# Kernel optimization log

Hardware: AMD Instinct MI355X
Metric: run time of the kernel (lower is better)

## Reference

```python
import jax, jax.numpy as jnp
import numpy as np

BS, M, CLIP_DIM = 64, 1000, 512
D = 512
N_WAYS = 20
N_Z = 8


def setup_inputs() -> dict:
    key = jax.random.key(0)
    ks = jax.random.split(key, 16)
    s = 0.02
    inp = {
        "x_context": jax.random.normal(ks[0], (BS, M, CLIP_DIM), jnp.float32),
        "y_context": jax.random.randint(ks[1], (BS, M), 0, N_WAYS),
        "x_query": jax.random.normal(ks[2], (BS, M, CLIP_DIM), jnp.float32),
        # image_proj
        "Wp": jax.random.normal(ks[3], (CLIP_DIM, D), jnp.float32) * s,
        "bp": jnp.zeros((D,), jnp.float32),
        # aggregator: Linear(d,d) -> GELU -> Linear(d,2d)
        "Wa1": jax.random.normal(ks[4], (D, D), jnp.float32) * s,
        "ba1": jnp.zeros((D,), jnp.float32),
        "Wa2": jax.random.normal(ks[5], (D, 2 * D), jnp.float32) * s,
        "ba2": jnp.zeros((2 * D,), jnp.float32),
        # decoder: Linear(d,d) -> GELU -> Linear(d,d)
        "Wd1": jax.random.normal(ks[6], (D, D), jnp.float32) * s,
        "bd1": jnp.zeros((D,), jnp.float32),
        "Wd2": jax.random.normal(ks[7], (D, D), jnp.float32) * s,
        "bd2": jnp.zeros((D,), jnp.float32),
    }
    return inp


def reference(x_context, y_context, x_query, Wp, bp, Wa1, ba1, Wa2, ba2, Wd1, bd1, Wd2, bd2):
    # project image embeddings: [bs, M, clip_dim] -> [bs, M, d]
    xc = x_context @ Wp + bp
    xq = x_query @ Wp + bp

    # encode_context_per_class: per-class masked sum == one-hot segment-sum
    # (original loops over classes doing (x*mask).sum(dim=1))
    oh = jax.nn.one_hot(y_context, N_WAYS, dtype=xc.dtype)  # [bs, M, N]
    r_C = jnp.einsum('bmn,bmd->bnd', oh, xc)  # [bs, N, d]

    # knowledge is None -> k = zeros; combined = relu(r + 0)
    combined = jax.nn.relu(r_C)
    h = jax.nn.gelu(combined @ Wa1 + ba1, approximate=False)
    stats = h @ Wa2 + ba2  # [bs, N, 2d]
    mu, scale_raw = stats[..., :D], stats[..., D:]
    scale = 0.01 + 0.99 * jax.nn.softplus(scale_raw)

    # eval path: sample n_z from q(z|C) via reparameterization
    eps = jax.random.normal(jax.random.key(42), (N_Z,) + mu.shape, mu.dtype)
    z_samples = mu[None] + scale[None] * eps  # [n_z, bs, N, d]

    # decode: class weight vectors then inner product with queries
    W = jax.nn.gelu(z_samples @ Wd1 + bd1, approximate=False) @ Wd2 + bd2
    logits = jnp.einsum('bqd,sbnd->sbqn', xq, W)  # [n_z, bs, Q*N, N]
    return logits, z_samples, mu, scale
```

## Files before the change

kernel.cpp:

```cpp
#include <hip/hip_runtime.h>
#include <hip/hip_bf16.h>
#include <stdint.h>


typedef __attribute__((ext_vector_type(8))) short short8;
typedef __attribute__((ext_vector_type(4))) float f32x4;

__device__ __forceinline__ float gelu_f(float x) {
    return 0.5f * x * (1.0f + erff(x * 0.70710678118654752440f));
}
__device__ __forceinline__ float softplus_f(float x) {
    return fmaxf(x, 0.0f) + log1pf(expf(-fabsf(x)));
}
__device__ __forceinline__ uint32_t cvt2(float a, float b) {
    __hip_bfloat162 h;
    h.x = __float2bfloat16(a);
    h.y = __float2bfloat16(b);
    uint32_t u; __builtin_memcpy(&u, &h, 4); return u;
}
__device__ __forceinline__ unsigned short f2bfu(float f) {
    __hip_bfloat16 h = __float2bfloat16(f);
    unsigned short u; __builtin_memcpy(&u, &h, 2); return u;
}
__device__ __forceinline__ float bfu2f(unsigned short u) {
    uint32_t v = (uint32_t)u << 16; float f; __builtin_memcpy(&f, &v, 4); return f;
}

__device__ __forceinline__ void threefry2x32(uint32_t k0, uint32_t k1,
                                             uint32_t x0, uint32_t x1,
                                             uint32_t& o0, uint32_t& o1) {
    uint32_t ks[3] = {k0, k1, k0 ^ k1 ^ 0x1BD11BDAu};
    x0 += ks[0]; x1 += ks[1];
    const uint32_t rot[8] = {13,15,26,6,17,29,16,24};
#pragma unroll
    for (int i = 0; i < 5; i++) {
#pragma unroll
        for (int j = 0; j < 4; j++) {
            uint32_t r = rot[(i & 1) * 4 + j];
            x0 += x1;
            x1 = (x1 << r) | (x1 >> (32 - r));
            x1 ^= x0;
        }
        x0 += ks[(i + 1) % 3];
        x1 += ks[(i + 2) % 3] + (uint32_t)(i + 1);
    }
    o0 = x0; o1 = x1;
}

__device__ __forceinline__ float bits_to_normal(uint32_t b) {
    float f = __uint_as_float((b >> 9) | 0x3F800000u) - 1.0f;
    const float lo = __uint_as_float(0xBF7FFFFFu);
    float u = fmaxf(lo, f * 2.0f + lo);
    return 1.41421356237309504880f * erfinvf(u);
}

__global__ __launch_bounds__(256) void po_k(
    const float* __restrict__ Wp, const float* __restrict__ Wa1,
    const float* __restrict__ Wa2, const float* __restrict__ Wd1,
    const float* __restrict__ Wd2, const float* __restrict__ bp,
    const float* __restrict__ bd2, const int* __restrict__ y,
    const float* __restrict__ xc,
    unsigned short* __restrict__ WpTb, unsigned short* __restrict__ Wa1Tb,
    unsigned short* __restrict__ Wa2Tb, unsigned short* __restrict__ WdT1b,
    unsigned short* __restrict__ Gtb,
    float* __restrict__ bv, float* __restrict__ w2bp,
    float* __restrict__ c0, float* __restrict__ cnt,
    float* __restrict__ Apart)
{
    __shared__ __align__(16) char sm[24576];
    __shared__ int lc[256];
    __shared__ float ws4[4];
    const int f = blockIdx.x;
    const int tid = threadIdx.x;

    if (f < 320) {
        float (*T)[65] = reinterpret_cast<float(*)[65]>(sm);
        const float* src; unsigned short* dst; int C, t, xb, yb;
        if (f < 64)       { src = Wp;  dst = WpTb;  C = 512;  t = f;       xb = t & 7;  yb = t >> 3; }
        else if (f < 128) { src = Wa1; dst = Wa1Tb; C = 512;  t = f - 64;  xb = t & 7;  yb = t >> 3; }
        else if (f < 256) { src = Wa2; dst = Wa2Tb; C = 1024; t = f - 128; xb = t & 15; yb = t >> 4; }
        else              { src = Wd1; dst = WdT1b; C = 512;  t = f - 256; xb = t & 7;  yb = t >> 3; }
        const int r0 = yb * 64, cc0 = xb * 64;
        const int rr = tid >> 4, cc = (tid & 15) * 4;
#pragma unroll
        for (int l = 0; l < 4; l++) {
            int row = rr + l * 16;
            float4 v = *(const float4*)&src[(size_t)(r0 + row) * C + cc0 + cc];
            T[row][cc] = v.x; T[row][cc+1] = v.y; T[row][cc+2] = v.z; T[row][cc+3] = v.w;
        }
        __syncthreads();
#pragma unroll
        for (int l = 0; l < 4; l++) {
            int n = rr + l * 16;
            uint2 u;
            u.x = cvt2(T[cc][n], T[cc+1][n]);
            u.y = cvt2(T[cc+2][n], T[cc+3][n]);
            *(uint2*)&dst[(size_t)(cc0 + n) * 512 + r0 + cc] = u;
        }
    } else if (f < 576) {
        const float* W = (f < 448) ? Wp : Wd2;
        const float* v = (f < 448) ? bd2 : bp;
        float* o = (f < 448) ? bv : w2bp;
        int t = (f < 448) ? f - 320 : f - 448;
        int wave = tid >> 6, lane = tid & 63;
        int r = t * 4 + wave;
        const float* row = W + (size_t)r * 512 + lane * 8;
        float4 x0 = *(const float4*)row;
        float4 x1 = *(const float4*)(row + 4);
        float4 v0 = *(const float4*)&v[lane * 8];
        float4 v1 = *(const float4*)&v[lane * 8 + 4];
        float s = x0.x*v0.x + x0.y*v0.y + x0.z*v0.z + x0.w*v0.w
                + x1.x*v1.x + x1.y*v1.y + x1.z*v1.z + x1.w*v1.w;
#pragma unroll
        for (int off = 32; off > 0; off >>= 1) s += __shfl_down(s, off, 64);
        if (lane == 0) o[r] = s;
    } else if (f == 576) {
        float s = bp[tid] * bd2[tid] + bp[tid + 256] * bd2[tid + 256];
#pragma unroll
        for (int off = 32; off > 0; off >>= 1) s += __shfl_down(s, off, 64);
        int wave = tid >> 6, lane = tid & 63;
        if (lane == 0) ws4[wave] = s;
        __syncthreads();
        if (tid == 0) c0[0] = ws4[0] + ws4[1] + ws4[2] + ws4[3];
    } else if (f < 641) {
        int b = f - 577;
        if (tid < 32) lc[tid] = 0;
        __syncthreads();
        for (int m = tid; m < 1000; m += 256)
            atomicAdd(&lc[y[b * 1000 + m]], 1);
        __syncthreads();
        if (tid < 20) cnt[b * 20 + tid] = (float)lc[tid];
    } else if (f < 673) {
        unsigned short* As = (unsigned short*)sm;
        unsigned short* Bs = (unsigned short*)(sm + 8192);
        const int g = f - 641;
        const int lane = tid & 63, w = tid >> 6;
        const int row0 = (g >> 2) * 64, col0 = (g & 3) * 128;
        f32x4 acc[4][2] = {};
        for (int k0 = 0; k0 < 512; k0 += 64) {
            {
                int row = tid >> 2, cs = (tid & 3) * 16;
                int swz = (row & 7) << 4;
                const float* src = Wp + (size_t)(row0 + row) * 512 + k0 + cs;
#pragma unroll
                for (int j = 0; j < 2; j++) {
                    float4 v0 = *(const float4*)(src + j * 8);
                    float4 v1 = *(const float4*)(src + j * 8 + 4);
                    uint4 u;
                    u.x = cvt2(v0.x, v0.y); u.y = cvt2(v0.z, v0.w);
                    u.z = cvt2(v1.x, v1.y); u.w = cvt2(v1.z, v1.w);
                    *(uint4*)((char*)As + row * 128 + (((cs + j * 8) * 2) ^ swz)) = u;
                }
            }
            {
                int row = tid >> 1, cs = (tid & 1) * 32;
                int swz = (row & 7) << 4;
                const float* src = Wd2 + (size_t)(col0 + row) * 512 + k0 + cs;
#pragma unroll
                for (int j = 0; j < 4; j++) {
                    float4 v0 = *(const float4*)(src + j * 8);
                    float4 v1 = *(const float4*)(src + j * 8 + 4);
                    uint4 u;
                    u.x = cvt2(v0.x, v0.y); u.y = cvt2(v0.z, v0.w);
                    u.z = cvt2(v1.x, v1.y); u.w = cvt2(v1.z, v1.w);
                    *(uint4*)((char*)Bs + row * 128 + (((cs + j * 8) * 2) ^ swz)) = u;
                }
            }
            __syncthreads();
#pragma unroll
            for (int ks = 0; ks < 2; ks++) {
                short8 a[4], bb[2];
#pragma unroll
                for (int mi = 0; mi < 4; mi++) {
                    int r = mi * 16 + (lane & 15);
                    a[mi] = *(const short8*)((const char*)As + r * 128 +
                              (((ks * 32 + (lane >> 4) * 8) * 2) ^ ((r & 7) << 4)));
                }
#pragma unroll
                for (int ni = 0; ni < 2; ni++) {
                    int n = w * 32 + ni * 16 + (lane & 15);
                    bb[ni] = *(const short8*)((const char*)Bs + n * 128 +
                              (((ks * 32 + (lane >> 4) * 8) * 2) ^ ((n & 7) << 4)));
                }
#pragma unroll
                for (int mi = 0; mi < 4; mi++)
#pragma unroll
                    for (int ni = 0; ni < 2; ni++)
                        acc[mi][ni] = __builtin_amdgcn_mfma_f32_16x16x32_bf16(a[mi], bb[ni], acc[mi][ni], 0, 0, 0);
            }
            __syncthreads();
        }
#pragma unroll
        for (int mi = 0; mi < 4; mi++)
#pragma unroll
            for (int ni = 0; ni < 2; ni++) {
                int c = col0 + w * 32 + ni * 16 + (lane & 15);
#pragma unroll
                for (int j = 0; j < 4; j++) {
                    int r = row0 + mi * 16 + (lane >> 4) * 4 + j;
                    Gtb[(size_t)r * 512 + c] = f2bfu(acc[mi][ni][j]);
                }
            }
    } else {
        unsigned short* Xs = (unsigned short*)sm;
        int* ys = lc;
        const int f2 = f - 673;
        const int chb = (f2 & 3) * 128;
        const int mc = (f2 >> 2) & 3;
        const int b = f2 >> 4;
        const int m00 = mc * 256;
        const int lane = tid & 63, w = tid >> 6;
        const int chs = w * 32;
        {
            int mg = m00 + tid;
            ys[tid] = (mg < 1000) ? y[b * 1000 + mg] : -1;
        }
        f32x4 acc[2][2] = {};
        for (int step = 0; step < 4; step++) {
            const int k0 = step * 64;
            int m = m00 + k0 + lane; if (m > 999) m = 999;
            const float* src = xc + ((size_t)b * 1000 + m) * 512 + chb + chs;
            float x[32];
#pragma unroll
            for (int j8 = 0; j8 < 8; j8++) {
                float4 v = *(const float4*)(src + j8 * 4);
                x[j8*4+0]=v.x; x[j8*4+1]=v.y; x[j8*4+2]=v.z; x[j8*4+3]=v.w;
            }
            __syncthreads();
#pragma unroll
            for (int j = 0; j < 32; j++) {
                int ch = chs + j;
                *(unsigned short*)((char*)Xs + ch * 128 + ((lane * 2) ^ ((ch & 7) << 4)))
                    = f2bfu(x[j]);
            }
            __syncthreads();
#pragma unroll
            for (int ks = 0; ks < 2; ks++) {
                int kb = ks * 32 + (lane >> 4) * 8;
                int4 yv0 = *(const int4*)&ys[k0 + kb];
                int4 yv1 = *(const int4*)&ys[k0 + kb + 4];
                int ya[8] = {yv0.x, yv0.y, yv0.z, yv0.w, yv1.x, yv1.y, yv1.z, yv1.w};
                short8 a[2];
#pragma unroll
                for (int mi = 0; mi < 2; mi++) {
                    int cls = mi * 16 + (lane & 15);
#pragma unroll
                    for (int e = 0; e < 8; e++)
                        a[mi][e] = (short)((ya[e] == cls) ? 0x3F80 : 0);
                }
                short8 bb[2];
#pragma unroll
                for (int ni = 0; ni < 2; ni++) {
                    int ch = chs + ni * 16 + (lane & 15);
                    bb[ni] = *(const short8*)((const char*)Xs + ch * 128 +
                               ((kb * 2) ^ ((ch & 7) << 4)));
                }
#pragma unroll
                for (int mi = 0; mi < 2; mi++)
#pragma unroll
                    for (int ni = 0; ni < 2; ni++)
                        acc[mi][ni] = __builtin_amdgcn_mfma_f32_16x16x32_bf16(a[mi], bb[ni], acc[mi][ni], 0, 0, 0);
            }
        }
        float* dst = Apart + (size_t)mc * 655360;
#pragma unroll
        for (int mi = 0; mi < 2; mi++) {
#pragma unroll
            for (int ni = 0; ni < 2; ni++) {
                int ch = chb + chs + ni * 16 + (lane & 15);
#pragma unroll
                for (int j = 0; j < 4; j++) {
                    int cls = mi * 16 + (lane >> 4) * 4 + j;
                    if (cls < 20)
                        dst[((size_t)b * 20 + cls) * 512 + ch] = acc[mi][ni][j];
                }
            }
        }
    }
}

template <int EPI, int MT, int A4>
__global__ __launch_bounds__(256) void gm2_k(const unsigned short* __restrict__ Abf,
                                             const unsigned short* __restrict__ Bbf,
                                             const float* __restrict__ bias,
                                             const float* __restrict__ extra,
                                             unsigned short* __restrict__ C0,
                                             float* __restrict__ F0,
                                             float* __restrict__ F1,
                                             int Nn) {
    __shared__ unsigned short As[MT * 64];
    __shared__ unsigned short Bs[128 * 64];
    const int tid = threadIdx.x;
    const int lane = tid & 63, w = tid >> 6;
    const int row0 = blockIdx.y * MT, col0 = blockIdx.x * 128;
    f32x4 acc[MT / 16][2] = {};
    for (int k0 = 0; k0 < 512; k0 += 64) {
        if constexpr (MT == 64) {
            int row = tid >> 2, cs = (tid & 3) * 16;
            int swz = (row & 7) << 4;
            const unsigned short* src = Abf + (size_t)(row0 + row) * 512 + k0 + cs;
#pragma unroll
            for (int j = 0; j < 2; j++) {
                uint4 u = *(const uint4*)(src + j * 8);
                *(uint4*)((char*)As + row * 128 + (((cs + j * 8) * 2) ^ swz)) = u;
            }
        } else {
            int row = tid >> 3, cs = (tid & 7) * 8;
            int swz = (row & 7) << 4;
            uint4 u;
            if constexpr (A4) {
                const float* p = (const float*)Abf + (size_t)(row0 + row) * 512 + k0 + cs;
                float4 s0 = *(const float4*)p;
                float4 s1 = *(const float4*)(p + 4);
#pragma unroll
                for (int q = 1; q < 4; q++) {
                    const float* pp = p + (size_t)q * 655360;
                    float4 v0 = *(const float4*)pp, v1 = *(const float4*)(pp + 4);
                    s0.x += v0.x; s0.y += v0.y; s0.z += v0.z; s0.w += v0.w;
                    s1.x += v1.x; s1.y += v1.y; s1.z += v1.z; s1.w += v1.w;
                }
                u.x = cvt2(s0.x, s0.y); u.y = cvt2(s0.z, s0.w);
                u.z = cvt2(s1.x, s1.y); u.w = cvt2(s1.z, s1.w);
            } else {
                u = *(const uint4*)(Abf + (size_t)(row0 + row) * 512 + k0 + cs);
            }
            *(uint4*)((char*)As + row * 128 + ((cs * 2) ^ swz)) = u;
        }
        {
            int row = tid >> 1, cs = (tid & 1) * 32;
            int swz = (row & 7) << 4;
            const unsigned short* src = Bbf + (size_t)(col0 + row) * 512 + k0 + cs;
#pragma unroll
            for (int j = 0; j < 4; j++) {
                uint4 u = *(const uint4*)(src + j * 8);
                *(uint4*)((char*)Bs + row * 128 + (((cs + j * 8) * 2) ^ swz)) = u;
            }
        }
        __syncthreads();
#pragma unroll
        for (int ks = 0; ks < 2; ks++) {
            short8 a[MT / 16], bb[2];
#pragma unroll
            for (int mi = 0; mi < MT / 16; mi++) {
                int r = mi * 16 + (lane & 15);
                a[mi] = *(const short8*)((const char*)As + r * 128 +
                          (((ks * 32 + (lane >> 4) * 8) * 2) ^ ((r & 7) << 4)));
            }
#pragma unroll
            for (int ni = 0; ni < 2; ni++) {
                int n = w * 32 + ni * 16 + (lane & 15);
                bb[ni] = *(const short8*)((const char*)Bs + n * 128 +
                          (((ks * 32 + (lane >> 4) * 8) * 2) ^ ((n & 7) << 4)));
            }
#pragma unroll
            for (int mi = 0; mi < MT / 16; mi++)
#pragma unroll
                for (int ni = 0; ni < 2; ni++)
                    acc[mi][ni] = __builtin_amdgcn_mfma_f32_16x16x32_bf16(a[mi], bb[ni], acc[mi][ni], 0, 0, 0);
        }
        __syncthreads();
    }
#pragma unroll
    for (int mi = 0; mi < MT / 16; mi++) {
#pragma unroll
        for (int ni = 0; ni < 2; ni++) {
            int c = col0 + w * 32 + ni * 16 + (lane & 15);
            float bvv = bias ? bias[c] : 0.f;
#pragma unroll
            for (int j = 0; j < 4; j++) {
                int r = row0 + mi * 16 + (lane >> 4) * 4 + j;
                float v = acc[mi][ni][j];
                if (EPI == 0) {
                    v += bvv;
                    C0[(size_t)r * Nn + c] = f2bfu(v);
                } else if (EPI == 1) {
                    v += extra[r] * bvv;
                    C0[(size_t)r * Nn + c] = f2bfu(fmaxf(v, 0.f));
                } else if (EPI == 2) {
                    C0[(size_t)r * Nn + c] = f2bfu(gelu_f(v + bvv));
                } else {
                    v += bvv;
                    if (c < 512) F0[(size_t)r * 512 + c] = v;
                    else F1[(size_t)r * 512 + (c - 512)] = 0.01f + 0.99f * softplus_f(v);
                }
            }
        }
    }
}

__global__ __launch_bounds__(256) void z2_k(const float* __restrict__ mu,
                                            const float* __restrict__ sc,
                                            float* __restrict__ z,
                                            unsigned short* __restrict__ zb) {
    const uint32_t NH = 2621440u;
    uint32_t i = blockIdx.x * 256u + threadIdx.x;
    if (i >= NH) return;
    uint32_t t0 = 2u * i;
    uint32_t o0, o1, p0, p1;
    threefry2x32(0u, 42u, 0u, t0, o0, o1);
    threefry2x32(0u, 42u, 0u, t0 + 1u, p0, p1);
    uint32_t r0 = t0 % 655360u;
    float2 mv = *(const float2*)&mu[r0];
    float2 sv = *(const float2*)&sc[r0];
    float z0 = mv.x + sv.x * bits_to_normal(o0 ^ o1);
    float z1 = mv.y + sv.y * bits_to_normal(p0 ^ p1);
    float2 zo; zo.x = z0; zo.y = z1;
    *(float2*)&z[t0] = zo;
    *(uint32_t*)&zb[t0] = cvt2(z0, z1);
}

__global__ __launch_bounds__(512) void wgv_k(const unsigned short* __restrict__ zb,
                                             const unsigned short* __restrict__ Wd1T,
                                             const unsigned short* __restrict__ Gt,
                                             const float* __restrict__ bd1,
                                             const float* __restrict__ bv,
                                             const float* __restrict__ w2bp,
                                             const float* __restrict__ c0,
                                             unsigned short* __restrict__ Vbf,
                                             float* __restrict__ beta) {
    __shared__ unsigned short Wg[64 * 512];
    __shared__ unsigned short As[64 * 64];
    const int r0 = blockIdx.x * 64;
    const int tid = threadIdx.x, lane = tid & 63, w = tid >> 6;
    const int col0 = w * 64;

    f32x4 acc[4][4] = {};
    for (int k0 = 0; k0 < 512; k0 += 64) {
        {
            int row = tid >> 3, cs = (tid & 7) * 8;
            int swz = (row & 7) << 4;
            uint4 u = *(const uint4*)(zb + (size_t)(r0 + row) * 512 + k0 + cs);
            *(uint4*)((char*)As + row * 128 + ((cs * 2) ^ swz)) = u;
        }
        __syncthreads();
#pragma unroll
        for (int ks = 0; ks < 2; ks++) {
            int kb = ks * 32 + (lane >> 4) * 8;
            short8 a[4], bb[4];
#pragma unroll
            for (int mi = 0; mi < 4; mi++) {
                int r = mi * 16 + (lane & 15);
                a[mi] = *(const short8*)((const char*)As + r * 128 +
                          ((kb * 2) ^ ((r & 7) << 4)));
            }
#pragma unroll
            for (int ni = 0; ni < 4; ni++) {
                int n = col0 + ni * 16 + (lane & 15);
                bb[ni] = *(const short8*)(Wd1T + (size_t)n * 512 + k0 + kb);
            }
#pragma unroll
            for (int mi = 0; mi < 4; mi++)
#pragma unroll
                for (int ni = 0; ni < 4; ni++)
                    acc[mi][ni] = __builtin_amdgcn_mfma_f32_16x16x32_bf16(a[mi], bb[ni], acc[mi][ni], 0, 0, 0);
        }
        __syncthreads();
    }
#pragma unroll
    for (int mi = 0; mi < 4; mi++) {
#pragma unroll
        for (int ni = 0; ni < 4; ni++) {
            int c = col0 + ni * 16 + (lane & 15);
            float bvv = bd1[c];
#pragma unroll
            for (int j = 0; j < 4; j++) {
                int r = mi * 16 + (lane >> 4) * 4 + j;
                float v = gelu_f(acc[mi][ni][j] + bvv);
                *(unsigned short*)((char*)Wg + r * 1024 + ((c * 2) ^ ((r & 7) << 4)))
                    = f2bfu(v);
            }
        }
    }
    __syncthreads();

    {
        int row = tid >> 3, p = tid & 7;
        const char* base = (const char*)Wg + row * 1024;
        int swz = (row & 7) << 4;
        float s = 0.f;
#pragma unroll
        for (int j = 0; j < 64; j++) {
            int c = p * 64 + j;
            s += bfu2f(*(const unsigned short*)(base + ((c * 2) ^ swz))) * w2bp[c];
        }
#pragma unroll
        for (int off = 4; off > 0; off >>= 1) s += __shfl_down(s, off, 64);
        if (p == 0) beta[r0 + row] = s + c0[0];
    }

    f32x4 acc2[4][4] = {};
    for (int k0 = 0; k0 < 512; k0 += 64) {
#pragma unroll
        for (int ks = 0; ks < 2; ks++) {
            int kb = ks * 32 + (lane >> 4) * 8;
            short8 a[4], bb[4];
#pragma unroll
            for (int mi = 0; mi < 4; mi++) {
                int r = mi * 16 + (lane & 15);
                a[mi] = *(const short8*)((const char*)Wg + r * 1024 +
                          (((k0 + kb) * 2) ^ ((r & 7) << 4)));
            }
#pragma unroll
            for (int ni = 0; ni < 4; ni++) {
                int n = col0 + ni * 16 + (lane & 15);
                bb[ni] = *(const short8*)(Gt + (size_t)n * 512 + k0 + kb);
            }
#pragma unroll
            for (int mi = 0; mi < 4; mi++)
#pragma unroll
                for (int ni = 0; ni < 4; ni++)
                    acc2[mi][ni] = __builtin_amdgcn_mfma_f32_16x16x32_bf16(a[mi], bb[ni], acc2[mi][ni], 0, 0, 0);
        }
    }
#pragma unroll
    for (int mi = 0; mi < 4; mi++) {
#pragma unroll
        for (int ni = 0; ni < 4; ni++) {
            int c = col0 + ni * 16 + (lane & 15);
            float bvv = bv[c];
#pragma unroll
            for (int j = 0; j < 4; j++) {
                int r = r0 + mi * 16 + (lane >> 4) * 4 + j;
                Vbf[(size_t)r * 512 + c] = f2bfu(acc2[mi][ni][j] + bvv);
            }
        }
    }
}

__global__ __launch_bounds__(512) void logits_mfma4_k(const float* __restrict__ Xq,
                                                      const unsigned short* __restrict__ Vb,
                                                      const float* __restrict__ beta,
                                                      float* __restrict__ out) {
    __shared__ unsigned short Vs[2][160 * 64];
    __shared__ float bs[160];
    const int u = blockIdx.x + 8 * blockIdx.y;
    const int xcd = u & 7, idx = u >> 3;
    const int b = (idx & 7) * 8 + xcd;
    const int qh = idx >> 3;
    const int tid = threadIdx.x, lane = tid & 63, w = tid >> 6;
    const int wq = w >> 1, wn = w & 1;

    if (tid < 160) {
        int s = tid / 20, n = tid - s * 20;
        bs[tid] = beta[(size_t)(s * 64 + b) * 20 + n];
    }

    auto stageV = [&](int buf, int k0) {
        for (int c = tid; c < 640; c += 512) {
            int row = c >> 2, off = (c & 3) * 32;
            int sdiv = row / 20;
            int row_g = row + sdiv * 1260 + b * 20;
            const unsigned short* src = Vb + (size_t)row_g * 512 + k0 + (c & 3) * 16;
            uint4 u0 = *(const uint4*)src;
            uint4 u1 = *(const uint4*)(src + 8);
            int swz = (row & 7) << 4;
            char* base = (char*)&Vs[buf][0] + row * 128;
            *(uint4*)(base + (off ^ swz)) = u0;
            *(uint4*)(base + ((off + 16) ^ swz)) = u1;
        }
    };

    const int klane = (lane >> 4) * 8;
    const float* xp[2];
    int qb[2];
#pragma unroll
    for (int qs = 0; qs < 2; qs++) {
        qb[qs] = qh * 128 + wq * 32 + qs * 16;
        int qr = qb[qs] + (lane & 15);
        if (qr > 999) qr = 999;
        xp[qs] = Xq + ((size_t)b * 1000 + qr) * 512 + klane;
    }
    int vrow[5], vswz[5];
#pragma unroll
    for (int nf = 0; nf < 5; nf++) {
        int rr = wn * 80 + nf * 16 + (lane & 15);
        vrow[nf] = rr * 128;
        vswz[nf] = (rr & 7) << 4;
    }

    stageV(0, 0);
    __syncthreads();

    f32x4 acc[2][5] = {};
    int cur = 0;
    for (int step = 0; step < 8; step++) {
        const int k0 = step * 64;
        if (step < 7) stageV(cur ^ 1, k0 + 64);
        const char* vbase = (const char*)&Vs[cur][0];
#pragma unroll
        for (int ks = 0; ks < 2; ks++) {
            int kb = (ks * 32 + klane) * 2;
            short8 bf[5];
#pragma unroll
            for (int nf = 0; nf < 5; nf++)
                bf[nf] = *(const short8*)(vbase + vrow[nf] + (kb ^ vswz[nf]));
            short8 af[2];
#pragma unroll
            for (int qs = 0; qs < 2; qs++) {
                const float* p = xp[qs] + k0 + ks * 32;
                float4 v0 = *(const float4*)p;
                float4 v1 = *(const float4*)(p + 4);
                uint4 uu;
                uu.x = cvt2(v0.x, v0.y); uu.y = cvt2(v0.z, v0.w);
                uu.z = cvt2(v1.x, v1.y); uu.w = cvt2(v1.z, v1.w);
                __builtin_memcpy(&af[qs], &uu, 16);
            }
#pragma unroll
            for (int qs = 0; qs < 2; qs++)
#pragma unroll
                for (int nf = 0; nf < 5; nf++)
                    acc[qs][nf] = __builtin_amdgcn_mfma_f32_16x16x32_bf16(af[qs], bf[nf], acc[qs][nf], 0, 0, 0);
        }
        __syncthreads();
        cur ^= 1;
    }

#pragma unroll
    for (int nf = 0; nf < 5; nf++) {
        int rl = wn * 80 + nf * 16 + (lane & 15);
        int s = rl / 20, n = rl - s * 20;
        float bb = bs[rl];
        size_t ob = (size_t)(s * 64 + b) * 20000;
#pragma unroll
        for (int qs = 0; qs < 2; qs++) {
#pragma unroll
            for (int j = 0; j < 4; j++) {
                int q = qb[qs] + (lane >> 4) * 4 + j;
                if (q < 1000)
                    out[ob + (size_t)q * 20 + n] = acc[qs][nf][j] + bb;
            }
        }
    }
}

extern "C" void kernel_launch(void* const* d_in, const int* in_sizes, int n_in,
                              void* d_out, int out_size, void* d_ws, size_t ws_size,
                              hipStream_t stream) {
    const float* x_context = (const float*)d_in[0];
    const int*   y_context = (const int*)d_in[1];
    const float* x_query   = (const float*)d_in[2];
    const float* Wp  = (const float*)d_in[3];
    const float* bp  = (const float*)d_in[4];
    const float* Wa1 = (const float*)d_in[5];
    const float* ba1 = (const float*)d_in[6];
    const float* Wa2 = (const float*)d_in[7];
    const float* ba2 = (const float*)d_in[8];
    const float* Wd1 = (const float*)d_in[9];
    const float* bd1 = (const float*)d_in[10];
    const float* Wd2 = (const float*)d_in[11];
    const float* bd2 = (const float*)d_in[12];

    float* out    = (float*)d_out;
    float* logits = out;
    float* z      = out + 10240000;
    float* mu     = out + 15482880;
    float* sc     = out + 16138240;

    float* ws   = (float*)d_ws;
    float* cnt  = ws;
    float* beta = cnt + 1280;
    float* bv   = beta + 10240;
    float* w2bp = bv + 512;
    float* c0   = w2bp + 512;
    unsigned short* WpTb  = (unsigned short*)(c0 + 63);
    unsigned short* Wa1Tb = WpTb + 262144;
    unsigned short* Wa2Tb = Wa1Tb + 262144;
    unsigned short* WdT1b = Wa2Tb + 524288;
    unsigned short* Gtb   = WdT1b + 262144;
    unsigned short* combb = Gtb + 262144;
    unsigned short* hb    = combb + 655360;
    unsigned short* zb    = hb + 655360;
    unsigned short* Vbf   = zb + 5242880;
    float* big = (float*)(Vbf + 5242880);

    po_k<<<dim3(1697), 256, 0, stream>>>(Wp, Wa1, Wa2, Wd1, Wd2, bp, bd2, y_context,
                                         x_context,
                                         WpTb, Wa1Tb, Wa2Tb, WdT1b, Gtb,
                                         bv, w2bp, c0, cnt, big);
    gm2_k<1, 32, 1><<<dim3(4, 40), 256, 0, stream>>>((const unsigned short*)big, WpTb, bp, cnt, combb, nullptr, nullptr, 512);
    gm2_k<2, 32, 0><<<dim3(4, 40), 256, 0, stream>>>(combb, Wa1Tb, ba1, nullptr, hb, nullptr, nullptr, 512);
    gm2_k<3, 32, 0><<<dim3(8, 40), 256, 0, stream>>>(hb, Wa2Tb, ba2, nullptr, nullptr, mu, sc, 1024);
    z2_k<<<dim3(10240), 256, 0, stream>>>(mu, sc, z, zb);
    wgv_k<<<dim3(160), 512, 0, stream>>>(zb, WdT1b, Gtb, bd1, bv, w2bp, c0, Vbf, beta);
    logits_mfma4_k<<<dim3(8, 64), 512, 0, stream>>>(x_query, Vbf, beta, logits);
}
```

Measured before the change: 216.1 us.

## Fuse projection, aggregator MLP and stats GEMMs into one chained kernel

Replaces three separate gm2_k launches (projection+relu, Wa1+GELU, Wa2+softplus) with a single chain_k kernel that keeps each 64-row tile's intermediate activations in shared memory across all three GEMMs. This removes two kernel launches and the global round trips of the combined and hidden bf16 buffers. In exchange only 20 blocks run, so the GPU is heavily underused, and B operands are read directly from global memory rather than staged in LDS.

```diff
diff --git a/kernel.cpp b/kernel.cpp
--- a/kernel.cpp
+++ b/kernel.cpp
@@ -279,37 +279,29 @@
     }
 }
 
-template <int EPI, int MT, int A4>
-__global__ __launch_bounds__(256) void gm2_k(const unsigned short* __restrict__ Abf,
-                                             const unsigned short* __restrict__ Bbf,
-                                             const float* __restrict__ bias,
-                                             const float* __restrict__ extra,
-                                             unsigned short* __restrict__ C0,
-                                             float* __restrict__ F0,
-                                             float* __restrict__ F1,
-                                             int Nn) {
-    __shared__ unsigned short As[MT * 64];
-    __shared__ unsigned short Bs[128 * 64];
-    const int tid = threadIdx.x;
-    const int lane = tid & 63, w = tid >> 6;
-    const int row0 = blockIdx.y * MT, col0 = blockIdx.x * 128;
-    f32x4 acc[MT / 16][2] = {};
-    for (int k0 = 0; k0 < 512; k0 += 64) {
-        if constexpr (MT == 64) {
-            int row = tid >> 2, cs = (tid & 3) * 16;
-            int swz = (row & 7) << 4;
-            const unsigned short* src = Abf + (size_t)(row0 + row) * 512 + k0 + cs;
-#pragma unroll
-            for (int j = 0; j < 2; j++) {
-                uint4 u = *(const uint4*)(src + j * 8);
-                *(uint4*)((char*)As + row * 128 + (((cs + j * 8) * 2) ^ swz)) = u;
-            }
-        } else {
-            int row = tid >> 3, cs = (tid & 7) * 8;
-            int swz = (row & 7) << 4;
-            uint4 u;
-            if constexpr (A4) {
-                const float* p = (const float*)Abf + (size_t)(row0 + row) * 512 + k0 + cs;
+__global__ __launch_bounds__(512) void chain_k(
+    const float* __restrict__ Apart,
+    const unsigned short* __restrict__ WpT,
+    const unsigned short* __restrict__ Wa1T,
+    const unsigned short* __restrict__ Wa2T,
+    const float* __restrict__ bp, const float* __restrict__ cnt,
+    const float* __restrict__ ba1, const float* __restrict__ ba2,
+    float* __restrict__ mu, float* __restrict__ sc)
+{
+    __shared__ unsigned short As[64 * 64];
+    __shared__ unsigned short Cw[64 * 512];
+    __shared__ unsigned short Hw[64 * 512];
+    const int r0 = blockIdx.x * 64;
+    const int tid = threadIdx.x, lane = tid & 63, w = tid >> 6;
+    const int col0 = w * 64;
+
+    {
+        f32x4 acc[4][4] = {};
+        for (int k0 = 0; k0 < 512; k0 += 64) {
+            {
+                int row = tid >> 3, cs = (tid & 7) * 8;
+                int swz = (row & 7) << 4;
+                const float* p = Apart + (size_t)(r0 + row) * 512 + k0 + cs;
                 float4 s0 = *(const float4*)p;
                 float4 s1 = *(const float4*)(p + 4);
 #pragma unroll
@@ -319,69 +311,137 @@
                     s0.x += v0.x; s0.y += v0.y; s0.z += v0.z; s0.w += v0.w;
                     s1.x += v1.x; s1.y += v1.y; s1.z += v1.z; s1.w += v1.w;
                 }
+                uint4 u;
                 u.x = cvt2(s0.x, s0.y); u.y = cvt2(s0.z, s0.w);
                 u.z = cvt2(s1.x, s1.y); u.w = cvt2(s1.z, s1.w);
-            } else {
-                u = *(const uint4*)(Abf + (size_t)(row0 + row) * 512 + k0 + cs);
-            }
-            *(uint4*)((char*)As + row * 128 + ((cs * 2) ^ swz)) = u;
-        }
-        {
-            int row = tid >> 1, cs = (tid & 1) * 32;
-            int swz = (row & 7) << 4;
-            const unsigned short* src = Bbf + (size_t)(col0 + row) * 512 + k0 + cs;
-#pragma unroll
-            for (int j = 0; j < 4; j++) {
-                uint4 u = *(const uint4*)(src + j * 8);
-                *(uint4*)((char*)Bs + row * 128 + (((cs + j * 8) * 2) ^ swz)) = u;
+                *(uint4*)((char*)As + row * 128 + ((cs * 2) ^ swz)) = u;
+            }
+            __syncthreads();
+#pragma unroll
+            for (int ks = 0; ks < 2; ks++) {
+                int kb = ks * 32 + (lane >> 4) * 8;
+                short8 a[4], bb[4];
+#pragma unroll
+                for (int mi = 0; mi < 4; mi++) {
+                    int r = mi * 16 + (lane & 15);
+                    a[mi] = *(const short8*)((const char*)As + r * 128 +
+                              ((kb * 2) ^ ((r & 7) << 4)));
+                }
+#pragma unroll
+                for (int ni = 0; ni < 4; ni++) {
+                    int n = col0 + ni * 16 + (lane & 15);
+                    bb[ni] = *(const short8*)(WpT + (size_t)n * 512 + k0 + kb);
+                }
+#pragma unroll
+                for (int mi = 0; mi < 4; mi++)
+#pragma unroll
+                    for (int ni = 0; ni < 4; ni++)
+                        acc[mi][ni] = __builtin_amdgcn_mfma_f32_16x16x32_bf16(a[mi], bb[ni], acc[mi][ni], 0, 0, 0);
+            }
+            __syncthreads();
+        }
+#pragma unroll
+        for (int mi = 0; mi < 4; mi++) {
+#pragma unroll
+            for (int ni = 0; ni < 4; ni++) {
+                int c = col0 + ni * 16 + (lane & 15);
+                float bpc = bp[c];
+#pragma unroll
+                for (int j = 0; j < 4; j++) {
+                    int r = mi * 16 + (lane >> 4) * 4 + j;
+                    float v = acc[mi][ni][j] + cnt[r0 + r] * bpc;
+                    *(unsigned short*)((char*)Cw + r * 1024 + ((c * 2) ^ ((r & 7) << 4)))
+                        = f2bfu(fmaxf(v, 0.f));
+                }
+            }
+        }
+    }
+    __syncthreads();
+
+    {
+        f32x4 acc[4][4] = {};
+        for (int k0 = 0; k0 < 512; k0 += 64) {
+#pragma unroll
+            for (int ks = 0; ks < 2; ks++) {
+                int kb = ks * 32 + (lane >> 4) * 8;
+                short8 a[4], bb[4];
+#pragma unroll
+                for (int mi = 0; mi < 4; mi++) {
+                    int r = mi * 16 + (lane & 15);
+                    a[mi] = *(const short8*)((const char*)Cw + r * 1024 +
+                              (((k0 + kb) * 2) ^ ((r & 7) << 4)));
+                }
+#pragma unroll
+                for (int ni = 0; ni < 4; ni++) {
+                    int n = col0 + ni * 16 + (lane & 15);
+                    bb[ni] = *(const short8*)(Wa1T + (size_t)n * 512 + k0 + kb);
+                }
+#pragma unroll
+                for (int mi = 0; mi < 4; mi++)
+#pragma unroll
+                    for (int ni = 0; ni < 4; ni++)
+                        acc[mi][ni] = __builtin_amdgcn_mfma_f32_16x16x32_bf16(a[mi], bb[ni], acc[mi][ni], 0, 0, 0);
             }
         }
         __syncthreads();
 #pragma unroll
-        for (int ks = 0; ks < 2; ks++) {
-            short8 a[MT / 16], bb[2];
-#pragma unroll
-            for (int mi = 0; mi < MT / 16; mi++) {
-                int r = mi * 16 + (lane & 15);
-                a[mi] = *(const short8*)((const char*)As + r * 128 +
-                          (((ks * 32 + (lane >> 4) * 8) * 2) ^ ((r & 7) << 4)));
-            }
-#pragma unroll
-            for (int ni = 0; ni < 2; ni++) {
-                int n = w * 32 + ni * 16 + (lane & 15);
-                bb[ni] = *(const short8*)((const char*)Bs + n * 128 +
-                          (((ks * 32 + (lane >> 4) * 8) * 2) ^ ((n & 7) << 4)));
-            }
-#pragma unroll
-            for (int mi = 0; mi < MT / 16; mi++)
-#pragma unroll
-                for (int ni = 0; ni < 2; ni++)
-                    acc[mi][ni] = __builtin_amdgcn_mfma_f32_16x16x32_bf16(a[mi], bb[ni], acc[mi][ni], 0, 0, 0);
-        }
-        __syncthreads();
-    }
-#pragma unroll
-    for (int mi = 0; mi < MT / 16; mi++) {
-#pragma unroll
-        for (int ni = 0; ni < 2; ni++) {
-            int c = col0 + w * 32 + ni * 16 + (lane & 15);
-            float bvv = bias ? bias[c] : 0.f;
-#pragma unroll
-            for (int j = 0; j < 4; j++) {
-                int r = row0 + mi * 16 + (lane >> 4) * 4 + j;
-                float v = acc[mi][ni][j];
-                if (EPI == 0) {
-                    v += bvv;
-                    C0[(size_t)r * Nn + c] = f2bfu(v);
-                } else if (EPI == 1) {
-                    v += extra[r] * bvv;
-                    C0[(size_t)r * Nn + c] = f2bfu(fmaxf(v, 0.f));
-                } else if (EPI == 2) {
-                    C0[(size_t)r * Nn + c] = f2bfu(gelu_f(v + bvv));
-                } else {
-                    v += bvv;
-                    if (c < 512) F0[(size_t)r * 512 + c] = v;
-                    else F1[(size_t)r * 512 + (c - 512)] = 0.01f + 0.99f * softplus_f(v);
+        for (int mi = 0; mi < 4; mi++) {
+#pragma unroll
+            for (int ni = 0; ni < 4; ni++) {
+                int c = col0 + ni * 16 + (lane & 15);
+                float bvv = ba1[c];
+#pragma unroll
+                for (int j = 0; j < 4; j++) {
+                    int r = mi * 16 + (lane >> 4) * 4 + j;
+                    float v = gelu_f(acc[mi][ni][j] + bvv);
+                    *(unsigned short*)((char*)Hw + r * 1024 + ((c * 2) ^ ((r & 7) << 4)))
+                        = f2bfu(v);
+                }
+            }
+        }
+    }
+    __syncthreads();
+
+#pragma unroll
+    for (int p = 0; p < 2; p++) {
+        f32x4 acc[4][4] = {};
+        const int cg0 = p * 512 + col0;
+        for (int k0 = 0; k0 < 512; k0 += 64) {
+#pragma unroll
+            for (int ks = 0; ks < 2; ks++) {
+                int kb = ks * 32 + (lane >> 4) * 8;
+                short8 a[4], bb[4];
+#pragma unroll
+                for (int mi = 0; mi < 4; mi++) {
+                    int r = mi * 16 + (lane & 15);
+                    a[mi] = *(const short8*)((const char*)Hw + r * 1024 +
+                              (((k0 + kb) * 2) ^ ((r & 7) << 4)));
+                }
+#pragma unroll
+                for (int ni = 0; ni < 4; ni++) {
+                    int n = cg0 + ni * 16 + (lane & 15);
+                    bb[ni] = *(const short8*)(Wa2T + (size_t)n * 512 + k0 + kb);
+                }
+#pragma unroll
+                for (int mi = 0; mi < 4; mi++)
+#pragma unroll
+                    for (int ni = 0; ni < 4; ni++)
+                        acc[mi][ni] = __builtin_amdgcn_mfma_f32_16x16x32_bf16(a[mi], bb[ni], acc[mi][ni], 0, 0, 0);
+            }
+        }
+#pragma unroll
+        for (int mi = 0; mi < 4; mi++) {
+#pragma unroll
+            for (int ni = 0; ni < 4; ni++) {
+                int cg = cg0 + ni * 16 + (lane & 15);
+                float bvv = ba2[cg];
+                int cl = cg - p * 512;
+#pragma unroll
+                for (int j = 0; j < 4; j++) {
+                    int r = r0 + mi * 16 + (lane >> 4) * 4 + j;
+                    float v = acc[mi][ni][j] + bvv;
+                    if (p == 0) mu[(size_t)r * 512 + cl] = v;
+                    else        sc[(size_t)r * 512 + cl] = 0.01f + 0.99f * softplus_f(v);
                 }
             }
         }
@@ -667,9 +727,7 @@
     unsigned short* Wa2Tb = Wa1Tb + 262144;
     unsigned short* WdT1b = Wa2Tb + 524288;
     unsigned short* Gtb   = WdT1b + 262144;
-    unsigned short* combb = Gtb + 262144;
-    unsigned short* hb    = combb + 655360;
-    unsigned short* zb    = hb + 655360;
+    unsigned short* zb    = Gtb + 262144;
     unsigned short* Vbf   = zb + 5242880;
     float* big = (float*)(Vbf + 5242880);
 
@@ -677,9 +735,8 @@
                                          x_context,
                                          WpTb, Wa1Tb, Wa2Tb, WdT1b, Gtb,
                                          bv, w2bp, c0, cnt, big);
-    gm2_k<1, 32, 1><<<dim3(4, 40), 256, 0, stream>>>((const unsigned short*)big, WpTb, bp, cnt, combb, nullptr, nullptr, 512);
-    gm2_k<2, 32, 0><<<dim3(4, 40), 256, 0, stream>>>(combb, Wa1Tb, ba1, nullptr, hb, nullptr, nullptr, 512);
-    gm2_k<3, 32, 0><<<dim3(8, 40), 256, 0, stream>>>(hb, Wa2Tb, ba2, nullptr, nullptr, mu, sc, 1024);
+    chain_k<<<dim3(20), 512, 0, stream>>>(big, WpTb, Wa1Tb, Wa2Tb,
+                                          bp, cnt, ba1, ba2, mu, sc);
     z2_k<<<dim3(10240), 256, 0, stream>>>(mu, sc, z, zb);
     wgv_k<<<dim3(160), 512, 0, stream>>>(zb, WdT1b, Gtb, bd1, bv, w2bp, c0, Vbf, beta);
     logits_mfma4_k<<<dim3(8, 64), 512, 0, stream>>>(x_query, Vbf, beta, logits);
```

After: 291.9 us. 35.0% more time.
